# Kernel optimization log

Measured on AMD Instinct MI355X. Metric: run time of the kernel, lower is better.

## Reference

```python
import jax, jax.numpy as jnp
import numpy as np
from jax import lax

B, H, W = 4, 512, 512
C_DOWN, C_UP = 256, 64
DH = DW = 32          # bottleneck feature map (H/16)
K = 512               # fixed proposal count per image (<= proposal_n_max)
NMS_THR = 0.2
MIN_DIST = 3
PROP_HALF = 5         # proposal_size(11) // 2
POOL = 7
NCLS = 4              # n_classes(3) + background


def leaky(x):
    return jnp.where(x > 0, x, 0.1 * x)


def setup_inputs() -> dict:
    key = jax.random.key(0)
    ks = jax.random.split(key, 12)
    s = lambda fan: np.float32(1.0 / np.sqrt(fan))
    return {
        "xhat": jax.random.uniform(ks[0], (B, 1, H, W), jnp.float32),
        "feat_down": jax.random.normal(ks[1], (B, C_DOWN, DH, DW), jnp.float32),
        "feat_up": jax.random.normal(ks[2], (B, C_UP, H, W), jnp.float32),
        # patch head: per-pixel => only 3x3 conv center taps contribute
        "pw1": jax.random.normal(ks[3], (256, C_DOWN), jnp.float32) * s(C_DOWN),
        "pb1": jnp.zeros((256,), jnp.float32),
        "pw2": jax.random.normal(ks[4], (256, 256), jnp.float32) * s(256),
        "pb2": jnp.zeros((256,), jnp.float32),
        "pw3": jax.random.normal(ks[5], (256, 256), jnp.float32) * s(256),
        "pb3": jnp.zeros((256,), jnp.float32),
        "pfc_w": jax.random.normal(ks[6], (2, 256), jnp.float32) * s(256),
        "pfc_b": jnp.zeros((2,), jnp.float32),
        # proposal head: full 3x3 convs on 7x7 pooled rois
        "qw1": jax.random.normal(ks[7], (256, C_UP, 3, 3), jnp.float32) * s(C_UP * 9),
        "qb1": jnp.zeros((256,), jnp.float32),
        "qw2": jax.random.normal(ks[8], (256, 256, 3, 3), jnp.float32) * s(256 * 9),
        "qb2": jnp.zeros((256,), jnp.float32),
        "qw3": jax.random.normal(ks[9], (256, 256, 3, 3), jnp.float32) * s(256 * 9),
        "qb3": jnp.zeros((256,), jnp.float32),
        "qfc_w": jax.random.normal(ks[10], (NCLS, 256), jnp.float32) * s(256),
        "qfc_b": jnp.zeros((NCLS,), jnp.float32),
    }


def reference(xhat, feat_down, feat_up, pw1, pb1, pw2, pb2, pw3, pb3, pfc_w, pfc_b,
              qw1, qb1, qw2, qb2, qw3, qb3, qfc_w, qfc_b):
    # ---- patch classifier applied per pixel (3x3 conv on 1x1 padded input == center tap)
    f = leaky(jnp.einsum('bchw,oc->bohw', feat_down, pw1) + pb1[None, :, None, None])
    f = leaky(jnp.einsum('bchw,oc->bohw', f, pw2) + pb2[None, :, None, None])
    f = leaky(jnp.einsum('bchw,oc->bohw', f, pw3) + pb3[None, :, None, None])
    plogits = jnp.einsum('bchw,oc->bohw', f, pfc_w) + pfc_b[None, :, None, None]
    patch_score = jax.nn.softmax(plogits, axis=1)[:, 1:2]                 # [B,1,DH,DW]
    patch_score = jax.image.resize(patch_score, (B, 1, H, W), 'bilinear')  # align_corners=False
    # gate belief map: bad pixels set to global mean of bad pixels
    bad = patch_score < 0.5
    nbad = jnp.maximum(jnp.sum(bad), 1).astype(xhat.dtype)
    mean_bad = jnp.sum(jnp.where(bad, xhat, 0.0)) / nbad
    bm = jnp.where(bad, mean_bad, xhat)[:, 0]                             # [B,H,W]
    # ---- belief-map NMS: local maxima above absolute threshold
    win = 2 * MIN_DIST + 1
    mp = lax.reduce_window(bm, -jnp.inf, lax.max, (1, win, win), (1, 1, 1), 'SAME')
    peak_scores = jnp.where((bm == mp) & (bm > NMS_THR), bm, -jnp.inf)
    top_s, top_i = lax.top_k(peak_scores.reshape(B, -1), K)               # [B,K]
    ys = (top_i // W).astype(jnp.int32)
    xs = (top_i % W).astype(jnp.int32)
    valid = top_s > NMS_THR
    coords = jnp.stack([xs, ys], axis=-1)                                 # (x, y)
    # ---- roi_align: 11x11 boxes around peaks, one bilinear sample per 7x7 bin center
    roi_size = 2.0 * PROP_HALF
    offs = (jnp.arange(POOL, dtype=jnp.float32) + 0.5) * (roi_size / POOL)
    px = (xs.astype(jnp.float32) - PROP_HALF)[..., None] + offs           # [B,K,7]
    py = (ys.astype(jnp.float32) - PROP_HALF)[..., None] + offs

    def sample_one(feat, py_i, px_i):
        # feat [C,H,W]; py_i/px_i [K,7] -> pooled [C,K,7,7]
        yy = jnp.broadcast_to(py_i[:, :, None], (K, POOL, POOL))
        xx = jnp.broadcast_to(px_i[:, None, :], (K, POOL, POOL))
        y0 = jnp.floor(yy); x0 = jnp.floor(xx)
        wy = yy - y0; wx = xx - x0
        y0i = jnp.clip(y0.astype(jnp.int32), 0, H - 1)
        y1i = jnp.clip(y0.astype(jnp.int32) + 1, 0, H - 1)
        x0i = jnp.clip(x0.astype(jnp.int32), 0, W - 1)
        x1i = jnp.clip(x0.astype(jnp.int32) + 1, 0, W - 1)
        g = lambda yi, xi: feat[:, yi, xi]
        return (g(y0i, x0i) * (1 - wy) * (1 - wx) + g(y0i, x1i) * (1 - wy) * wx
                + g(y1i, x0i) * wy * (1 - wx) + g(y1i, x1i) * wy * wx)

    pooled = jax.vmap(sample_one)(feat_up, py, px)                        # [B,C,K,7,7]
    pooled = pooled.transpose(0, 2, 1, 3, 4).reshape(B * K, C_UP, POOL, POOL)
    # ---- proposal classifier head
    dn = ('NCHW', 'OIHW', 'NCHW')
    h = leaky(lax.conv_general_dilated(pooled, qw1, (1, 1), 'SAME', dimension_numbers=dn) + qb1[None, :, None, None])
    h = leaky(lax.conv_general_dilated(h, qw2, (1, 1), 'SAME', dimension_numbers=dn) + qb2[None, :, None, None])
    h = leaky(lax.conv_general_dilated(h, qw3, (1, 1), 'SAME', dimension_numbers=dn) + qb3[None, :, None, None])
    h = jnp.max(h, axis=(2, 3))                                           # AdaptiveMaxPool2d(1)
    cls_logits = (h @ qfc_w.T + qfc_b).reshape(B, K, NCLS)
    return cls_logits, coords, top_s, valid
```

## Files before the change

kernel.cpp:

```cpp
#include <hip/hip_runtime.h>
#include <math.h>

typedef _Float16 half_t;
typedef half_t half8 __attribute__((ext_vector_type(8)));
typedef half_t half4 __attribute__((ext_vector_type(4)));
typedef float  f32x16 __attribute__((ext_vector_type(16)));
typedef double dbl2  __attribute__((ext_vector_type(2)));

#define BB 4
#define HH 512
#define WW 512
#define IMGPIX (HH*WW)
#define KSEL 512
#define NPROP (BB*KSEL)
#define CUP 64
#define NMS_THR 0.2f

#define OFF_S32    0
#define OFF_SUM    32768
#define OFF_CNT    32776
#define OFF_CCNT   32784
#define OFF_HIST   32800
#define ZERO_BASE  32768
#define ZERO_LEN   262176
#define OFF_PFX    294944
#define OFF_R      294976
#define OFF_BITMAP 295040
#define OFF_KEYS   426112
#define OFF_SEL    8814720
#define OFF_PROPS  8831104
#define OFF_W1     8847488
#define OFF_W2     9142400
#define OFF_W3     10322048

#define LRELU_F(x) ((x) > 0.0f ? (x) : 0.1f*(x))

__global__ __launch_bounds__(256) void repatch_k(
    const float* __restrict__ fdown,
    const float* __restrict__ pw1, const float* __restrict__ pb1,
    const float* __restrict__ pw2, const float* __restrict__ pb2,
    const float* __restrict__ pw3, const float* __restrict__ pb3,
    const float* __restrict__ pfcw, const float* __restrict__ pfcb,
    double* __restrict__ s32,
    const float* __restrict__ qw1, const float* __restrict__ qw2,
    const float* __restrict__ qw3,
    half_t* __restrict__ W1, half_t* __restrict__ W2, half_t* __restrict__ W3)
{
  if (blockIdx.x >= 512) {
    const int tot1 = 256*64*9, tot2 = 256*256*9;
    int idx = (blockIdx.x - 512)*256 + threadIdx.x;
    const float* src; half_t* dst; int IC, KS, l;
    if (idx < tot1)              { src = qw1; dst = W1; IC = 64;  KS = 4;  l = idx; }
    else if (idx < tot1 + tot2)  { src = qw2; dst = W2; IC = 256; KS = 16; l = idx - tot1; }
    else if (idx < tot1 + 2*tot2){ src = qw3; dst = W3; IC = 256; KS = 16; l = idx - tot1 - tot2; }
    else return;
    int tap = l % 9;
    int t   = l / 9;
    int ic  = t % IC;
    int oc  = t / IC;
    int ks  = ic >> 4, kin = ic & 15;
    dst[((size_t)(tap*KS + ks)*256 + oc)*16 + kin] = (half_t)src[l];
    return;
  }
  __shared__ __align__(16) double xb[8][256];
  const int t = threadIdx.x;
  const int base_px = blockIdx.x * 8;
#pragma unroll
  for (int p = 0; p < 8; ++p) {
    int px = base_px + p;
    int b = px >> 10, rem = px & 1023;
    xb[p][t] = (double)fdown[(size_t)(b*256 + t)*1024 + rem];
  }
  __syncthreads();
  const float* Ws[3] = {pw1, pw2, pw3};
  const float* Bs[3] = {pb1, pb2, pb3};
  for (int L = 0; L < 3; ++L) {
    double acc[8];
    double bias = (double)Bs[L][t];
#pragma unroll
    for (int p = 0; p < 8; ++p) acc[p] = bias;
    const float* wrow = Ws[L] + t*256;
    for (int c = 0; c < 256; c += 2) {
      double w0 = (double)wrow[c], w1 = (double)wrow[c+1];
#pragma unroll
      for (int p = 0; p < 8; ++p) {
        dbl2 xv = *(const dbl2*)&xb[p][c];
        acc[p] += w0 * xv.x;
        acc[p] += w1 * xv.y;
      }
    }
    __syncthreads();
#pragma unroll
    for (int p = 0; p < 8; ++p)
      xb[p][t] = acc[p] > 0.0 ? acc[p] : 0.1*acc[p];
    __syncthreads();
  }
  if (t < 8) {
    double l0 = (double)pfcb[0], l1 = (double)pfcb[1];
    for (int c = 0; c < 256; ++c) {
      double xv = xb[t][c];
      l0 += (double)pfcw[c]       * xv;
      l1 += (double)pfcw[256 + c] * xv;
    }
    double m  = fmax(l0, l1);
    double e0 = exp(l0 - m), e1 = exp(l1 - m);
    s32[base_px + t] = e1 / (e0 + e1);
  }
}

__device__ __forceinline__ double upsample_ps(const double* __restrict__ s32,
                                              int b, int oy, int ox)
{
  double sy = (oy + 0.5)*0.0625 - 0.5;
  double sx = (ox + 0.5)*0.0625 - 0.5;
  double fy = floor(sy), fx = floor(sx);
  double wy = sy - fy,   wx = sx - fx;
  int y0 = (int)fy, x0 = (int)fx;
  int y0i = min(max(y0,   0), 31), y1i = min(max(y0+1, 0), 31);
  int x0i = min(max(x0,   0), 31), x1i = min(max(x0+1, 0), 31);
  const double* s = s32 + b*1024;
  double v00 = s[y0i*32+x0i], v01 = s[y0i*32+x1i];
  double v10 = s[y1i*32+x0i], v11 = s[y1i*32+x1i];
  return v00*(1.0-wy)*(1.0-wx) + v01*(1.0-wy)*wx
       + v10*wy*(1.0-wx)       + v11*wy*wx;
}

__global__ __launch_bounds__(256) void mean_k(
    const float* __restrict__ xhat, const double* __restrict__ s32,
    double* __restrict__ sum, unsigned long long* __restrict__ cnt,
    unsigned long long* __restrict__ bitmap)
{
  int id = blockIdx.x*256 + threadIdx.x;
  int b = id >> 18, rem = id & (IMGPIX-1);
  int oy = rem >> 9, ox = rem & 511;
  double ps = upsample_ps(s32, b, oy, ox);
  bool bad = ps < 0.5;
  int lane = threadIdx.x & 63;
  unsigned long long bb = __ballot(bad);
  if (lane == 0) bitmap[id >> 6] = bb;
  double v = bad ? (double)xhat[id] : 0.0;
  int    c = bad ? 1 : 0;
  for (int off = 32; off; off >>= 1) {
    v += __shfl_down(v, off);
    c += __shfl_down(c, off);
  }
  __shared__ double sv[4];
  __shared__ int    sc[4];
  int w = threadIdx.x >> 6;
  if (lane == 0) { sv[w] = v; sc[w] = c; }
  __syncthreads();
  if (threadIdx.x == 0) {
    atomicAdd(sum, sv[0]+sv[1]+sv[2]+sv[3]);
    atomicAdd(cnt, (unsigned long long)(sc[0]+sc[1]+sc[2]+sc[3]));
  }
}

__global__ __launch_bounds__(512) void keyfuse_k(
    const float* __restrict__ xhat, const unsigned long long* __restrict__ bitmap,
    const double* __restrict__ sum, const unsigned long long* __restrict__ cnt,
    unsigned long long* __restrict__ keys, unsigned int* __restrict__ hist0)
{
  __shared__ float rowm[14][512];
  __shared__ float bmv[8][512];
  __shared__ float rt[512];
  __shared__ unsigned int lh[4096];
  const int tid = threadIdx.x;
  const int img = blockIdx.x >> 6;
  const int rb  = (blockIdx.x & 63) * 8;
  for (int i = tid; i < 4096; i += 512) lh[i] = 0;

  unsigned long long n = *cnt; if (n < 1) n = 1;
  const float mean = (float)(*sum / (double)n);
  const int ibase = img * IMGPIX;

  for (int r = 0; r < 14; ++r) {
    int y = rb - 3 + r;
    float v = -INFINITY;
    if (y >= 0 && y < 512) {
      int id = ibase + (y << 9) + tid;
      bool bad = (bitmap[id >> 6] >> (id & 63)) & 1ull;
      v = bad ? mean : xhat[id];
    }
    int cr = y - rb;
    if (cr >= 0 && cr < 8) bmv[cr][tid] = v;
    rt[tid] = v;
    __syncthreads();
    int lo = max(tid-3, 0), hi = min(tid+3, 511);
    float m = rt[lo];
    for (int xx = lo+1; xx <= hi; ++xx) m = fmaxf(m, rt[xx]);
    rowm[r][tid] = m;
    __syncthreads();
  }

  const int lane = tid & 63;
  for (int yy = 0; yy < 8; ++yy) {
    float mp = rowm[yy][tid];
#pragma unroll
    for (int d = 1; d < 7; ++d) mp = fmaxf(mp, rowm[yy + d][tid]);
    float v = bmv[yy][tid];
    bool cand = (v == mp) && (v > NMS_THR);
    int rem = ((rb + yy) << 9) + tid;
    unsigned int inv = (unsigned int)((IMGPIX-1) - rem);
    unsigned long long key = cand
        ? ((((unsigned long long)__float_as_uint(v)) << 18) | inv)
        : (unsigned long long)inv;
    keys[ibase + rem] = key;
    int bin = (int)(key >> 36);
    unsigned long long active = ~0ull;
    while (active) {
      int src = __ffsll((long long)active) - 1;
      int bsel = __shfl(bin, src);
      unsigned long long match = __ballot(bin == bsel) & active;
      if (lane == src) atomicAdd(&lh[bsel], (unsigned int)__popcll(match));
      active &= ~match;
    }
  }
  __syncthreads();
  for (int i = tid; i < 4096; i += 512)
    if (lh[i]) atomicAdd(&hist0[img*4096 + i], lh[i]);
}

__global__ __launch_bounds__(512) void hist_k(
    const unsigned long long* __restrict__ keys,
    const unsigned long long* __restrict__ pfx,
    unsigned int* __restrict__ hist, int shift)
{
  __shared__ unsigned int lh[4096];
  const int tid = threadIdx.x;
  for (int i = tid; i < 4096; i += 512) lh[i] = 0;
  int id = blockIdx.x*512 + tid;
  int img = blockIdx.x >> 9;
  unsigned long long key = keys[id];
  bool pred = (key >> (shift + 12)) == pfx[img];
  int bin = (int)((unsigned int)(key >> shift) & 4095u);
  __syncthreads();
  int lane = tid & 63;
  unsigned long long active = __ballot(pred);
  while (active) {
    int src = __ffsll((long long)active) - 1;
    int bsel = __shfl(bin, src);
    unsigned long long match = __ballot(bin == bsel) & active;
    if (lane == src) atomicAdd(&lh[bsel], (unsigned int)__popcll(match));
    active &= ~match;
  }
  __syncthreads();
  for (int i = tid; i < 4096; i += 512)
    if (lh[i]) atomicAdd(&hist[img*4096 + i], lh[i]);
}

__global__ __launch_bounds__(512) void scan_k(
    const unsigned int* __restrict__ hist,
    unsigned long long* __restrict__ pfx, unsigned int* __restrict__ Rbuf,
    int pass)
{
  __shared__ unsigned int lsA[512], lsB[512];
  const int b = blockIdx.x, tid = threadIdx.x;
  unsigned long long pin = (pass == 0) ? 0ull : pfx[b];
  unsigned int Rin = (pass == 0) ? (unsigned int)KSEL : Rbuf[b];
  const unsigned int* h = hist + b*4096;
  unsigned int v[8]; unsigned int loc = 0;
#pragma unroll
  for (int j = 0; j < 8; ++j) { v[j] = h[tid*8 + j]; loc += v[j]; }
  lsA[tid] = loc;
  __syncthreads();
  unsigned int* s = lsA; unsigned int* d = lsB;
  for (int dd = 1; dd < 512; dd <<= 1) {
    unsigned int val = s[tid] + ((tid + dd < 512) ? s[tid + dd] : 0u);
    d[tid] = val;
    __syncthreads();
    unsigned int* t = s; s = d; d = t;
  }
  unsigned int nxt = (tid + 1 < 512) ? s[tid + 1] : 0u;
#pragma unroll
  for (int j = 7; j >= 0; --j) {
    unsigned int sfx = nxt + v[j];
    if (sfx >= Rin && nxt < Rin) {
      pfx[b] = (pin << 12) | (unsigned long long)(unsigned int)(tid*8 + j);
      Rbuf[b] = Rin - nxt;
    }
    nxt = sfx;
  }
}

__global__ __launch_bounds__(512) void collect_k(
    const unsigned long long* __restrict__ keys,
    const unsigned long long* __restrict__ pfx,
    unsigned int* __restrict__ ccnt, unsigned long long* __restrict__ sel)
{
  int id = blockIdx.x*512 + threadIdx.x;
  int img = blockIdx.x >> 9;
  unsigned long long key = keys[id];
  if (key >= pfx[img]) {
    unsigned int pos = atomicAdd(&ccnt[img], 1u);
    if (pos < 512) sel[img*512 + pos] = key;
  }
}

__global__ __launch_bounds__(512) void sortout_k(
    const unsigned long long* __restrict__ sel,
    float* __restrict__ out, int* __restrict__ props)
{
  __shared__ unsigned long long s[512];
  const int b = blockIdx.x, tid = threadIdx.x;
  s[tid] = sel[b*512 + tid];
  __syncthreads();
  for (int size = 2; size <= 512; size <<= 1) {
    for (int stride = size >> 1; stride > 0; stride >>= 1) {
      int j = tid ^ stride;
      if (j > tid) {
        unsigned long long a = s[tid], c = s[j];
        bool up = ((tid & size) == 0);
        if (up ? (a < c) : (a > c)) { s[tid] = c; s[j] = a; }
      }
      __syncthreads();
    }
  }
  unsigned long long k = s[tid];
  unsigned int fbits = (unsigned int)(k >> 18);
  int idx = (IMGPIX-1) - (int)(k & 0x3FFFFull);
  int y = idx >> 9, x = idx & 511;
  float val = fbits ? __uint_as_float(fbits) : -INFINITY;
  int slot = (b << 9) + tid;
  out[12288 + slot]       = val;
  out[8192 + slot*2 + 0]  = (float)x;
  out[8192 + slot*2 + 1]  = (float)y;
  out[14336 + slot]       = (val > NMS_THR) ? 1.0f : 0.0f;
  props[slot*2 + 0] = x;
  props[slot*2 + 1] = y;
}

#define SA2 264
#define SA1 72
#define ZROW 49

template<int KS, int SA>
__device__ __forceinline__ void conv32(
    const half_t* __restrict__ Wl, const half_t* __restrict__ Xin,
    int mtb, int l31, int lh, f32x16 acc[2][2])
{
#pragma unroll
  for (int mt = 0; mt < 2; ++mt)
#pragma unroll
    for (int nt = 0; nt < 2; ++nt)
#pragma unroll
      for (int r = 0; r < 16; ++r) acc[mt][nt][r] = 0.f;

  for (int tap = 0; tap < 9; ++tap) {
    const int dy = tap/3 - 1, dx = tap%3 - 1;
    int xb[2];
#pragma unroll
    for (int nt = 0; nt < 2; ++nt) {
      int px = nt*32 + l31;
      int y = px/7, x = px - y*7;
      int yy = y + dy, xx = x + dx;
      bool valid = (px < 49) & (yy >= 0) & (yy < 7) & (xx >= 0) & (xx < 7);
      int row = valid ? (yy*7 + xx) : ZROW;
      xb[nt] = row*SA + lh*8;
    }
    const half_t* wb = Wl + ((size_t)(tap*KS)*256 + mtb + l31)*16 + lh*8;
#pragma unroll 4
    for (int ks = 0; ks < KS; ++ks) {
      half8 b0 = *(const half8*)(Xin + xb[0] + ks*16);
      half8 b1 = *(const half8*)(Xin + xb[1] + ks*16);
      half8 a0 = *(const half8*)(wb + (ks*256      )*16);
      half8 a1 = *(const half8*)(wb + (ks*256 + 32 )*16);
      acc[0][0] = __builtin_amdgcn_mfma_f32_32x32x16_f16(a0, b0, acc[0][0], 0,0,0);
      acc[0][1] = __builtin_amdgcn_mfma_f32_32x32x16_f16(a0, b1, acc[0][1], 0,0,0);
      acc[1][0] = __builtin_amdgcn_mfma_f32_32x32x16_f16(a1, b0, acc[1][0], 0,0,0);
      acc[1][1] = __builtin_amdgcn_mfma_f32_32x32x16_f16(a1, b1, acc[1][1], 0,0,0);
    }
  }
}

__device__ __forceinline__ void store32(
    half_t* __restrict__ X2, const float* __restrict__ bias,
    int mtb, int ntb, int l31, int lh, const f32x16& a)
{
  int px = ntb + l31;
  if (px >= 49) return;
  half_t* dst = X2 + px*SA2;
  int oc0 = mtb + 4*lh;
#pragma unroll
  for (int q = 0; q < 4; ++q) {
    int oc = oc0 + 8*q;
    half4 h;
#pragma unroll
    for (int r = 0; r < 4; ++r) {
      float v = a[4*q + r] + bias[oc + r];
      h[r] = (half_t)LRELU_F(v);
    }
    *(half4*)(dst + oc) = h;
  }
}

__global__ __launch_bounds__(256, 4) void head_k(
    const float* __restrict__ fup, const int* __restrict__ props,
    const half_t* __restrict__ W1, const half_t* __restrict__ W2,
    const half_t* __restrict__ W3,
    const float* __restrict__ qb1, const float* __restrict__ qb2,
    const float* __restrict__ qb3,
    const float* __restrict__ qfcw, const float* __restrict__ qfcb,
    float* __restrict__ out)
{
  __shared__ __align__(16) half_t X2[50*SA2];
  __shared__ __align__(16) char  U[50*SA1*2];
  half_t* X1 = (half_t*)U;
  float*  S  = (float*)U;

  const int p  = blockIdx.x;
  const int b  = p >> 9;
  const int tid = threadIdx.x;
  const int w = tid >> 6, lane = tid & 63;
  const int l31 = lane & 31, lh = lane >> 5;
  const int mtb = w*64;

  for (int i = tid; i < SA2; i += 256) X2[ZROW*SA2 + i] = (half_t)0.f;
  for (int i = tid; i < SA1; i += 256) X1[ZROW*SA1 + i] = (half_t)0.f;

  const float step = (float)(10.0/7.0);
  const int cx = props[2*p], cy = props[2*p+1];
  for (int it = tid; it < CUP*49; it += 256) {
    int c = it / 49, bin = it - c*49;
    int iy = bin / 7, ix = bin - iy*7;
    float fy = ((float)cy - 5.0f) + ((float)iy + 0.5f)*step;
    float fx = ((float)cx - 5.0f) + ((float)ix + 0.5f)*step;
    float y0f = floorf(fy), x0f = floorf(fx);
    float wy = fy - y0f,    wx = fx - x0f;
    int y0 = (int)y0f, x0 = (int)x0f;
    int y0i = min(max(y0,   0), 511), y1i = min(max(y0+1, 0), 511);
    int x0i = min(max(x0,   0), 511), x1i = min(max(x0+1, 0), 511);
    const float* f = fup + ((size_t)(b*CUP + c) << 18);
    float v00 = f[(y0i<<9)+x0i], v01 = f[(y0i<<9)+x1i];
    float v10 = f[(y1i<<9)+x0i], v11 = f[(y1i<<9)+x1i];
    float v = v00*(1.f-wy)*(1.f-wx) + v01*(1.f-wy)*wx
            + v10*wy*(1.f-wx)       + v11*wy*wx;
    X1[(iy*7 + ix)*SA1 + c] = (half_t)v;
  }
  __syncthreads();

  f32x16 acc[2][2];

  conv32<4, SA1>(W1, X1, mtb, l31, lh, acc);
#pragma unroll
  for (int mt = 0; mt < 2; ++mt)
#pragma unroll
    for (int nt = 0; nt < 2; ++nt)
      store32(X2, qb1, mtb + mt*32, nt*32, l31, lh, acc[mt][nt]);
  __syncthreads();

  conv32<16, SA2>(W2, X2, mtb, l31, lh, acc);
  __syncthreads();
#pragma unroll
  for (int mt = 0; mt < 2; ++mt)
#pragma unroll
    for (int nt = 0; nt < 2; ++nt)
      store32(X2, qb2, mtb + mt*32, nt*32, l31, lh, acc[mt][nt]);
  __syncthreads();

  conv32<16, SA2>(W3, X2, mtb, l31, lh, acc);
#pragma unroll
  for (int mt = 0; mt < 2; ++mt) {
#pragma unroll
    for (int q = 0; q < 4; ++q) {
#pragma unroll
      for (int r = 0; r < 4; ++r) {
        int oc = mtb + mt*32 + 8*q + 4*lh + r;
        float bv = qb3[oc];
        float m = LRELU_F(acc[mt][0][4*q + r] + bv);
        if (l31 < 17) {
          float v2 = LRELU_F(acc[mt][1][4*q + r] + bv);
          m = fmaxf(m, v2);
        }
#pragma unroll
        for (int d = 1; d < 32; d <<= 1) m = fmaxf(m, __shfl_xor(m, d));
        if (l31 == 0) S[oc] = m;
      }
    }
  }
  __syncthreads();

  float* P = S + 256;
  {
    float h = S[tid];
#pragma unroll
    for (int j = 0; j < 4; ++j) P[j*256 + tid] = h * qfcw[j*256 + tid];
  }
  __syncthreads();
  {
    int j = tid >> 6, o = tid & 63;
    float v = P[j*256 + o] + P[j*256 + o + 64]
            + P[j*256 + o + 128] + P[j*256 + o + 192];
#pragma unroll
    for (int d = 1; d < 64; d <<= 1) v += __shfl_xor(v, d);
    if (o == 0) out[p*4 + j] = v + qfcb[j];
  }
}

extern "C" void kernel_launch(void* const* d_in, const int* in_sizes, int n_in,
                              void* d_out, int out_size, void* d_ws, size_t ws_size,
                              hipStream_t stream)
{
  (void)in_sizes; (void)n_in; (void)out_size; (void)ws_size;
  const float* xhat  = (const float*)d_in[0];
  const float* fdown = (const float*)d_in[1];
  const float* fup   = (const float*)d_in[2];
  const float* pw1   = (const float*)d_in[3];
  const float* pb1   = (const float*)d_in[4];
  const float* pw2   = (const float*)d_in[5];
  const float* pb2   = (const float*)d_in[6];
  const float* pw3   = (const float*)d_in[7];
  const float* pb3   = (const float*)d_in[8];
  const float* pfcw  = (const float*)d_in[9];
  const float* pfcb  = (const float*)d_in[10];
  const float* qw1   = (const float*)d_in[11];
  const float* qb1   = (const float*)d_in[12];
  const float* qw2   = (const float*)d_in[13];
  const float* qb2   = (const float*)d_in[14];
  const float* qw3   = (const float*)d_in[15];
  const float* qb3   = (const float*)d_in[16];
  const float* qfcw  = (const float*)d_in[17];
  const float* qfcb  = (const float*)d_in[18];

  char* ws = (char*)d_ws;
  double*             s32   = (double*)(ws + OFF_S32);
  double*             sum   = (double*)(ws + OFF_SUM);
  unsigned long long* cnt   = (unsigned long long*)(ws + OFF_CNT);
  unsigned int*       ccnt  = (unsigned int*)(ws + OFF_CCNT);
  unsigned int*       hist  = (unsigned int*)(ws + OFF_HIST);
  unsigned long long* pfx   = (unsigned long long*)(ws + OFF_PFX);
  unsigned int*       Rbuf  = (unsigned int*)(ws + OFF_R);
  unsigned long long* bmap  = (unsigned long long*)(ws + OFF_BITMAP);
  unsigned long long* keys  = (unsigned long long*)(ws + OFF_KEYS);
  unsigned long long* sel   = (unsigned long long*)(ws + OFF_SEL);
  int*                props = (int*)(ws + OFF_PROPS);
  half_t*             Wp1   = (half_t*)(ws + OFF_W1);
  half_t*             Wp2   = (half_t*)(ws + OFF_W2);
  half_t*             Wp3   = (half_t*)(ws + OFF_W3);
  float*              out   = (float*)d_out;

  hipMemsetAsync(ws + ZERO_BASE, 0, ZERO_LEN, stream);

  const int repack_blocks = (256*64*9 + 2*256*256*9 + 255)/256;
  repatch_k<<<512 + repack_blocks, 256, 0, stream>>>(
      fdown, pw1,pb1, pw2,pb2, pw3,pb3, pfcw,pfcb, s32,
      qw1, qw2, qw3, Wp1, Wp2, Wp3);

  mean_k   <<<4096, 256, 0, stream>>>(xhat, s32, sum, cnt, bmap);
  keyfuse_k<<<256, 512, 0, stream>>>(xhat, bmap, sum, cnt, keys, hist + 0*4*4096);
  scan_k   <<<BB, 512, 0, stream>>>(hist + 0*4*4096, pfx, Rbuf, 0);
  hist_k   <<<2048, 512, 0, stream>>>(keys, pfx, hist + 1*4*4096, 24);
  scan_k   <<<BB, 512, 0, stream>>>(hist + 1*4*4096, pfx, Rbuf, 1);
  hist_k   <<<2048, 512, 0, stream>>>(keys, pfx, hist + 2*4*4096, 12);
  scan_k   <<<BB, 512, 0, stream>>>(hist + 2*4*4096, pfx, Rbuf, 2);
  hist_k   <<<2048, 512, 0, stream>>>(keys, pfx, hist + 3*4*4096, 0);
  scan_k   <<<BB, 512, 0, stream>>>(hist + 3*4*4096, pfx, Rbuf, 3);
  collect_k<<<2048, 512, 0, stream>>>(keys, pfx, ccnt, sel);
  sortout_k<<<BB, 512, 0, stream>>>(sel, out, props);

  head_k   <<<NPROP, 256, 0, stream>>>(fup, props, Wp1, Wp2, Wp3,
                                       qb1, qb2, qb3, qfcw, qfcb, out);
}
```

Baseline: 950.8 us.

## Compact candidates in keyfuse and fuse radix select, collect, and sort per image

Keyfuse now writes only NMS candidates, plus the first image row as filler, into a compacted per-image buffer through wave-aggregated atomics, instead of writing keys for every pixel and building a histogram. A single select_k kernel per image then runs the four 12-bit radix-select passes, the collection and the bitonic sort in shared memory. This removes nine launches and three full-image histogram sweeps, and shrinks the memset. The weight repack also now writes half4 vectors. The risk is that only four blocks do the selection, which serialises if candidate counts are large.

```diff
diff --git a/kernel.cpp b/kernel.cpp
--- a/kernel.cpp
+++ b/kernel.cpp
@@ -20,18 +20,17 @@
 #define OFF_SUM    32768
 #define OFF_CNT    32776
 #define OFF_CCNT   32784
-#define OFF_HIST   32800
 #define ZERO_BASE  32768
-#define ZERO_LEN   262176
-#define OFF_PFX    294944
-#define OFF_R      294976
+#define ZERO_LEN   32
 #define OFF_BITMAP 295040
-#define OFF_KEYS   426112
+#define OFF_CAND   426112
 #define OFF_SEL    8814720
 #define OFF_PROPS  8831104
 #define OFF_W1     8847488
 #define OFF_W2     9142400
 #define OFF_W3     10322048
+
+#define CANDCAP (1u<<18)
 
 #define LRELU_F(x) ((x) > 0.0f ? (x) : 0.1f*(x))
 
@@ -47,19 +46,27 @@
     half_t* __restrict__ W1, half_t* __restrict__ W2, half_t* __restrict__ W3)
 {
   if (blockIdx.x >= 512) {
-    const int tot1 = 256*64*9, tot2 = 256*256*9;
-    int idx = (blockIdx.x - 512)*256 + threadIdx.x;
-    const float* src; half_t* dst; int IC, KS, l;
-    if (idx < tot1)              { src = qw1; dst = W1; IC = 64;  KS = 4;  l = idx; }
-    else if (idx < tot1 + tot2)  { src = qw2; dst = W2; IC = 256; KS = 16; l = idx - tot1; }
-    else if (idx < tot1 + 2*tot2){ src = qw3; dst = W3; IC = 256; KS = 16; l = idx - tot1 - tot2; }
+    const int tot1q = (256*64*9*16/16)/4;
+    const int tot2q = (256*256*9*16/16)/4;
+    int g = (blockIdx.x - 512)*256 + threadIdx.x;
+    const float* src; half_t* dst; int IC, KS, q;
+    if (g < tot1q)               { src = qw1; dst = W1; IC = 64;  KS = 4;  q = g; }
+    else if (g < tot1q + tot2q)  { src = qw2; dst = W2; IC = 256; KS = 16; q = g - tot1q; }
+    else if (g < tot1q + 2*tot2q){ src = qw3; dst = W3; IC = 256; KS = 16; q = g - tot1q - tot2q; }
     else return;
-    int tap = l % 9;
-    int t   = l / 9;
-    int ic  = t % IC;
-    int oc  = t / IC;
-    int ks  = ic >> 4, kin = ic & 15;
-    dst[((size_t)(tap*KS + ks)*256 + oc)*16 + kin] = (half_t)src[l];
+    int o4  = q*4;
+    int kin = o4 & 15;
+    int t   = o4 >> 4;
+    int oc  = t & 255;
+    int r   = t >> 8;
+    int ks  = r % KS, tap = r / KS;
+    half4 h;
+#pragma unroll
+    for (int j = 0; j < 4; ++j) {
+      int ic = ks*16 + kin + j;
+      h[j] = (half_t)src[(oc*IC + ic)*9 + tap];
+    }
+    *(half4*)(dst + o4) = h;
     return;
   }
   __shared__ __align__(16) double xb[8][256];
@@ -158,16 +165,14 @@
 __global__ __launch_bounds__(512) void keyfuse_k(
     const float* __restrict__ xhat, const unsigned long long* __restrict__ bitmap,
     const double* __restrict__ sum, const unsigned long long* __restrict__ cnt,
-    unsigned long long* __restrict__ keys, unsigned int* __restrict__ hist0)
+    unsigned long long* __restrict__ candbuf, unsigned int* __restrict__ ccnt)
 {
   __shared__ float rowm[14][512];
   __shared__ float bmv[8][512];
   __shared__ float rt[512];
-  __shared__ unsigned int lh[4096];
   const int tid = threadIdx.x;
   const int img = blockIdx.x >> 6;
   const int rb  = (blockIdx.x & 63) * 8;
-  for (int i = tid; i < 4096; i += 512) lh[i] = 0;
 
   unsigned long long n = *cnt; if (n < 1) n = 1;
   const float mean = (float)(*sum / (double)n);
@@ -193,6 +198,7 @@
   }
 
   const int lane = tid & 63;
+  unsigned long long* cb = candbuf + ((size_t)img << 18);
   for (int yy = 0; yy < 8; ++yy) {
     float mp = rowm[yy][tid];
 #pragma unroll
@@ -204,118 +210,111 @@
     unsigned long long key = cand
         ? ((((unsigned long long)__float_as_uint(v)) << 18) | inv)
         : (unsigned long long)inv;
-    keys[ibase + rem] = key;
-    int bin = (int)(key >> 36);
-    unsigned long long active = ~0ull;
-    while (active) {
-      int src = __ffsll((long long)active) - 1;
-      int bsel = __shfl(bin, src);
-      unsigned long long match = __ballot(bin == bsel) & active;
-      if (lane == src) atomicAdd(&lh[bsel], (unsigned int)__popcll(match));
-      active &= ~match;
-    }
-  }
-  __syncthreads();
-  for (int i = tid; i < 4096; i += 512)
-    if (lh[i]) atomicAdd(&hist0[img*4096 + i], lh[i]);
-}
-
-__global__ __launch_bounds__(512) void hist_k(
-    const unsigned long long* __restrict__ keys,
-    const unsigned long long* __restrict__ pfx,
-    unsigned int* __restrict__ hist, int shift)
+    bool keep = cand | (rem < 512);
+    unsigned long long m = __ballot(keep);
+    int c = __popcll(m);
+    if (c) {
+      int leader = __ffsll((long long)m) - 1;
+      unsigned base = 0;
+      if (lane == leader) base = atomicAdd(&ccnt[img], (unsigned)c);
+      base = __shfl(base, leader);
+      if (keep) {
+        unsigned rk = (unsigned)__popcll(m & ((1ull << lane) - 1ull));
+        cb[base + rk] = key;
+      }
+    }
+  }
+}
+
+__global__ __launch_bounds__(512) void select_k(
+    const unsigned long long* __restrict__ candbuf,
+    const unsigned int* __restrict__ ccnt,
+    float* __restrict__ out, int* __restrict__ props)
 {
   __shared__ unsigned int lh[4096];
-  const int tid = threadIdx.x;
-  for (int i = tid; i < 4096; i += 512) lh[i] = 0;
-  int id = blockIdx.x*512 + tid;
-  int img = blockIdx.x >> 9;
-  unsigned long long key = keys[id];
-  bool pred = (key >> (shift + 12)) == pfx[img];
-  int bin = (int)((unsigned int)(key >> shift) & 4095u);
-  __syncthreads();
-  int lane = tid & 63;
-  unsigned long long active = __ballot(pred);
-  while (active) {
-    int src = __ffsll((long long)active) - 1;
-    int bsel = __shfl(bin, src);
-    unsigned long long match = __ballot(bin == bsel) & active;
-    if (lane == src) atomicAdd(&lh[bsel], (unsigned int)__popcll(match));
-    active &= ~match;
-  }
-  __syncthreads();
-  for (int i = tid; i < 4096; i += 512)
-    if (lh[i]) atomicAdd(&hist[img*4096 + i], lh[i]);
-}
-
-__global__ __launch_bounds__(512) void scan_k(
-    const unsigned int* __restrict__ hist,
-    unsigned long long* __restrict__ pfx, unsigned int* __restrict__ Rbuf,
-    int pass)
-{
   __shared__ unsigned int lsA[512], lsB[512];
+  __shared__ unsigned long long sel[512];
+  __shared__ unsigned long long pfx_s;
+  __shared__ unsigned int R_s, cnt_s;
+
   const int b = blockIdx.x, tid = threadIdx.x;
-  unsigned long long pin = (pass == 0) ? 0ull : pfx[b];
-  unsigned int Rin = (pass == 0) ? (unsigned int)KSEL : Rbuf[b];
-  const unsigned int* h = hist + b*4096;
-  unsigned int v[8]; unsigned int loc = 0;
-#pragma unroll
-  for (int j = 0; j < 8; ++j) { v[j] = h[tid*8 + j]; loc += v[j]; }
-  lsA[tid] = loc;
-  __syncthreads();
-  unsigned int* s = lsA; unsigned int* d = lsB;
-  for (int dd = 1; dd < 512; dd <<= 1) {
-    unsigned int val = s[tid] + ((tid + dd < 512) ? s[tid + dd] : 0u);
-    d[tid] = val;
-    __syncthreads();
-    unsigned int* t = s; s = d; d = t;
-  }
-  unsigned int nxt = (tid + 1 < 512) ? s[tid + 1] : 0u;
-#pragma unroll
-  for (int j = 7; j >= 0; --j) {
-    unsigned int sfx = nxt + v[j];
-    if (sfx >= Rin && nxt < Rin) {
-      pfx[b] = (pin << 12) | (unsigned long long)(unsigned int)(tid*8 + j);
-      Rbuf[b] = Rin - nxt;
-    }
-    nxt = sfx;
-  }
-}
-
-__global__ __launch_bounds__(512) void collect_k(
-    const unsigned long long* __restrict__ keys,
-    const unsigned long long* __restrict__ pfx,
-    unsigned int* __restrict__ ccnt, unsigned long long* __restrict__ sel)
-{
-  int id = blockIdx.x*512 + threadIdx.x;
-  int img = blockIdx.x >> 9;
-  unsigned long long key = keys[id];
-  if (key >= pfx[img]) {
-    unsigned int pos = atomicAdd(&ccnt[img], 1u);
-    if (pos < 512) sel[img*512 + pos] = key;
-  }
-}
-
-__global__ __launch_bounds__(512) void sortout_k(
-    const unsigned long long* __restrict__ sel,
-    float* __restrict__ out, int* __restrict__ props)
-{
-  __shared__ unsigned long long s[512];
-  const int b = blockIdx.x, tid = threadIdx.x;
-  s[tid] = sel[b*512 + tid];
-  __syncthreads();
+  const int lane = tid & 63;
+  const unsigned long long* cb = candbuf + ((size_t)b << 18);
+  unsigned int n = ccnt[b]; if (n > CANDCAP) n = CANDCAP;
+
+  if (tid == 0) { pfx_s = 0ull; R_s = (unsigned)KSEL; cnt_s = 0u; }
+  __syncthreads();
+
+  for (int pass = 0; pass < 4; ++pass) {
+    const int shift = 36 - 12*pass;
+    const unsigned long long pfxv = pfx_s;
+    const unsigned int Rv = R_s;
+    for (int i = tid; i < 4096; i += 512) lh[i] = 0;
+    __syncthreads();
+
+    for (unsigned i0 = 0; i0 < n; i0 += 512) {
+      unsigned i = i0 + tid;
+      unsigned long long k = (i < n) ? cb[i] : 0ull;
+      bool pred = (i < n) && (pass == 0 || (k >> (shift + 12)) == pfxv);
+      int bin = (int)((unsigned)(k >> shift) & 4095u);
+      unsigned long long active = __ballot(pred);
+      while (active) {
+        int src = __ffsll((long long)active) - 1;
+        int bsel = __shfl(bin, src);
+        unsigned long long match = __ballot(bin == bsel) & active;
+        if (lane == src) atomicAdd(&lh[bsel], (unsigned)__popcll(match));
+        active &= ~match;
+      }
+    }
+    __syncthreads();
+
+    unsigned v[8]; unsigned loc = 0;
+#pragma unroll
+    for (int j = 0; j < 8; ++j) { v[j] = lh[tid*8 + j]; loc += v[j]; }
+    lsA[tid] = loc;
+    __syncthreads();
+    unsigned* s = lsA; unsigned* d = lsB;
+    for (int dd = 1; dd < 512; dd <<= 1) {
+      unsigned val = s[tid] + ((tid + dd < 512) ? s[tid + dd] : 0u);
+      d[tid] = val;
+      __syncthreads();
+      unsigned* t = s; s = d; d = t;
+    }
+    unsigned nxt = (tid + 1 < 512) ? s[tid + 1] : 0u;
+#pragma unroll
+    for (int j = 7; j >= 0; --j) {
+      unsigned sfx = nxt + v[j];
+      if (sfx >= Rv && nxt < Rv) {
+        pfx_s = (pfxv << 12) | (unsigned long long)(unsigned)(tid*8 + j);
+        R_s = Rv - nxt;
+      }
+      nxt = sfx;
+    }
+    __syncthreads();
+  }
+
+  const unsigned long long cut = pfx_s;
+  for (unsigned i = tid; i < n; i += 512) {
+    unsigned long long k = cb[i];
+    if (k >= cut) {
+      unsigned pos = atomicAdd(&cnt_s, 1u);
+      if (pos < 512) sel[pos] = k;
+    }
+  }
+  __syncthreads();
+
   for (int size = 2; size <= 512; size <<= 1) {
     for (int stride = size >> 1; stride > 0; stride >>= 1) {
       int j = tid ^ stride;
       if (j > tid) {
-        unsigned long long a = s[tid], c = s[j];
+        unsigned long long a = sel[tid], c = sel[j];
         bool up = ((tid & size) == 0);
-        if (up ? (a < c) : (a > c)) { s[tid] = c; s[j] = a; }
+        if (up ? (a < c) : (a > c)) { sel[tid] = c; sel[j] = a; }
       }
       __syncthreads();
     }
   }
-  unsigned long long k = s[tid];
+  unsigned long long k = sel[tid];
   unsigned int fbits = (unsigned int)(k >> 18);
   int idx = (IMGPIX-1) - (int)(k & 0x3FFFFull);
   int y = idx >> 9, x = idx & 511;
@@ -526,12 +525,8 @@
   double*             sum   = (double*)(ws + OFF_SUM);
   unsigned long long* cnt   = (unsigned long long*)(ws + OFF_CNT);
   unsigned int*       ccnt  = (unsigned int*)(ws + OFF_CCNT);
-  unsigned int*       hist  = (unsigned int*)(ws + OFF_HIST);
-  unsigned long long* pfx   = (unsigned long long*)(ws + OFF_PFX);
-  unsigned int*       Rbuf  = (unsigned int*)(ws + OFF_R);
   unsigned long long* bmap  = (unsigned long long*)(ws + OFF_BITMAP);
-  unsigned long long* keys  = (unsigned long long*)(ws + OFF_KEYS);
-  unsigned long long* sel   = (unsigned long long*)(ws + OFF_SEL);
+  unsigned long long* cand  = (unsigned long long*)(ws + OFF_CAND);
   int*                props = (int*)(ws + OFF_PROPS);
   half_t*             Wp1   = (half_t*)(ws + OFF_W1);
   half_t*             Wp2   = (half_t*)(ws + OFF_W2);
@@ -540,23 +535,14 @@
 
   hipMemsetAsync(ws + ZERO_BASE, 0, ZERO_LEN, stream);
 
-  const int repack_blocks = (256*64*9 + 2*256*256*9 + 255)/256;
+  const int repack_blocks = (36864 + 2*147456 + 255)/256;
   repatch_k<<<512 + repack_blocks, 256, 0, stream>>>(
       fdown, pw1,pb1, pw2,pb2, pw3,pb3, pfcw,pfcb, s32,
       qw1, qw2, qw3, Wp1, Wp2, Wp3);
 
   mean_k   <<<4096, 256, 0, stream>>>(xhat, s32, sum, cnt, bmap);
-  keyfuse_k<<<256, 512, 0, stream>>>(xhat, bmap, sum, cnt, keys, hist + 0*4*4096);
-  scan_k   <<<BB, 512, 0, stream>>>(hist + 0*4*4096, pfx, Rbuf, 0);
-  hist_k   <<<2048, 512, 0, stream>>>(keys, pfx, hist + 1*4*4096, 24);
-  scan_k   <<<BB, 512, 0, stream>>>(hist + 1*4*4096, pfx, Rbuf, 1);
-  hist_k   <<<2048, 512, 0, stream>>>(keys, pfx, hist + 2*4*4096, 12);
-  scan_k   <<<BB, 512, 0, stream>>>(hist + 2*4*4096, pfx, Rbuf, 2);
-  hist_k   <<<2048, 512, 0, stream>>>(keys, pfx, hist + 3*4*4096, 0);
-  scan_k   <<<BB, 512, 0, stream>>>(hist + 3*4*4096, pfx, Rbuf, 3);
-  collect_k<<<2048, 512, 0, stream>>>(keys, pfx, ccnt, sel);
-  sortout_k<<<BB, 512, 0, stream>>>(sel, out, props);
-
+  keyfuse_k<<<256, 512, 0, stream>>>(xhat, bmap, sum, cnt, cand, ccnt);
+  select_k <<<BB, 512, 0, stream>>>(cand, ccnt, out, props);
   head_k   <<<NPROP, 256, 0, stream>>>(fup, props, Wp1, Wp2, Wp3,
                                        qb1, qb2, qb3, qfcw, qfcb, out);
 }
```

New measurement: 1.394 ms. 46.6% more time.
